# Performance work log

Measured on AMD Instinct MI355X. Metric: run time of the kernel, lower is better.

## Reference

```python
import jax, jax.numpy as jnp
import numpy as np
from jax import lax

B, N, F = 4, 8192, 64      # clouds, points per cloud, feature dim
RATIO = 0.25
M = int(N * RATIO)
K = 32                      # max_num_neighbors (torch_geometric radius default)
R = 0.1                     # ball radius (unit-cube points -> ~32 nbrs expected)
H = 64                      # MLP hidden/output width


def setup_inputs() -> dict:
    key = jax.random.key(0)
    k1, k2, k3, k4, k5, k6 = jax.random.split(key, 6)
    x = jax.random.normal(k1, (B * N, F), jnp.float32)
    pos = jax.random.uniform(k2, (B * N, 3), jnp.float32)  # unit cube
    batch = jnp.repeat(jnp.arange(B, dtype=jnp.int32), N)  # contiguous cloud ids
    s1 = 1.0 / np.sqrt(F + 3)
    W1 = jax.random.uniform(k3, (F + 3, H), jnp.float32, -s1, s1)
    b1 = jax.random.uniform(k4, (H,), jnp.float32, -s1, s1)
    s2 = 1.0 / np.sqrt(H)
    W2 = jax.random.uniform(k5, (H, H), jnp.float32, -s2, s2)
    b2 = jax.random.uniform(k6, (H,), jnp.float32, -s2, s2)
    return {"x": x, "pos": pos, "batch": batch,
            "W1": W1, "b1": b1, "W2": W2, "b2": b2}


def _fps(pc):
    """Farthest point sampling on one cloud pc [N,3] -> [M] int32 indices.
    Deterministic start at index 0 (torch_geometric uses a random start)."""
    d0 = jnp.full((N,), jnp.inf, pc.dtype)

    def step(carry, _):
        dist, last = carry
        d = jnp.sum((pc - pc[last]) ** 2, axis=-1)
        dist = jnp.minimum(dist, d)
        nxt = jnp.argmax(dist).astype(jnp.int32)
        return (dist, nxt), last

    _, idx = lax.scan(step, (d0, jnp.int32(0)), None, length=M)
    return idx


def _radius_knn(pc, centers):
    """Up-to-K neighbors of each center within radius R (nearest-first).
    Returns nbr_idx [M,K] and validity mask [M,K]."""
    d2 = jnp.sum((centers[:, None, :] - pc[None, :, :]) ** 2, axis=-1)  # [M,N]
    masked = jnp.where(d2 <= R * R, d2, jnp.inf)
    negd, idx = lax.top_k(-masked, K)
    return idx, negd > -jnp.inf


def reference(x, pos, batch, W1, b1, W2, b2):
    # batch ids are contiguous with equal-sized clouds -> reshape to [B,N,...]
    xb = x.reshape(B, N, F)
    pb = pos.reshape(B, N, 3)

    def per_cloud(xc, pc):
        samp = _fps(pc)                        # [M]   FPS indices
        centers = pc[samp]                     # [M,3]
        nbr, mask = _radius_knn(pc, centers)   # [M,K]
        # PointConv message: MLP(concat[x_j, pos_j - pos_i])
        feat = jnp.concatenate(
            [xc[nbr], pc[nbr] - centers[:, None, :]], axis=-1)  # [M,K,F+3]
        h = jax.nn.relu(feat @ W1 + b1)
        h = jax.nn.relu(h @ W2 + b2)           # [M,K,H]
        h = jnp.where(mask[..., None], h, -jnp.inf)
        out = jnp.max(h, axis=1)               # max aggregation over neighbors
        out = jnp.where(jnp.isfinite(out), out, 0.0)
        return out, centers

    out, centers = jax.vmap(per_cloud)(xb, pb)
    new_batch = jnp.repeat(jnp.arange(B, dtype=jnp.int32), M)
    return out.reshape(B * M, H), centers.reshape(B * M, 3), new_batch
```

## Files before the change

### kernel.cpp

```cpp
#include <hip/hip_runtime.h>
#include <hip/hip_bf16.h>
#include <float.h>
#include <math.h>

#define NB 4
#define NN 8192
#define FF 64
#define MM 2048
#define KK 32
#define HH 64

#define FT 512

typedef float v2f __attribute__((ext_vector_type(2)));

#define DPP_FMAX(v, ctrl, rmask)                                                \
    { int _t = __builtin_amdgcn_update_dpp((int)0xff800000, __float_as_int(v),  \
                   (ctrl), (rmask), 0xf, false);                                \
      (v) = fmaxf((v), __int_as_float(_t)); }
#define DPP_FMAX6(v)  DPP_FMAX(v,0x111,0xf) DPP_FMAX(v,0x112,0xf) \
                      DPP_FMAX(v,0x114,0xf) DPP_FMAX(v,0x118,0xf) \
                      DPP_FMAX(v,0x142,0xa) DPP_FMAX(v,0x143,0xc)

#define DPP_IMIN(v, ctrl, rmask)                                                \
    { int _t = __builtin_amdgcn_update_dpp((int)0x7fffffff, (v),                \
                   (ctrl), (rmask), 0xf, false);                                \
      (v) = min((v), _t); }
#define DPP_IMIN6(v)  DPP_IMIN(v,0x111,0xf) DPP_IMIN(v,0x112,0xf) \
                      DPP_IMIN(v,0x114,0xf) DPP_IMIN(v,0x118,0xf) \
                      DPP_IMIN(v,0x142,0xa) DPP_IMIN(v,0x143,0xc)

__global__ __launch_bounds__(FT) void fps_kernel(
    const float* __restrict__ pos,
    int* __restrict__ samp,
    float* __restrict__ centers_out,
    float* __restrict__ batch_out)
{
#pragma clang fp contract(off)
    __shared__ float4 pts4[NN];
    __shared__ float vslot[2][8];
    __shared__ int   islot[2][8];

    const int b = blockIdx.x;
    const float* pb = pos + (size_t)b * NN * 3;
    const int tid = threadIdx.x;
    const int w   = tid >> 6;
    const int lane = tid & 63;

    for (int j = tid; j < NN; j += FT)
        pts4[j] = make_float4(pb[j * 3 + 0], pb[j * 3 + 1], pb[j * 3 + 2], 0.0f);
    for (int j = tid; j < MM; j += FT) batch_out[b * MM + j] = (float)b;
    __syncthreads();

    v2f pxv[8], pyv[8], pzv[8], dv[8];
#pragma unroll
    for (int j = 0; j < 8; ++j) {
        const float4 p0 = pts4[(2 * j) * FT + tid];
        const float4 p1 = pts4[(2 * j + 1) * FT + tid];
        pxv[j] = (v2f){p0.x, p1.x};
        pyv[j] = (v2f){p0.y, p1.y};
        pzv[j] = (v2f){p0.z, p1.z};
        dv[j]  = (v2f){INFINITY, INFINITY};
    }

    int   cur = 0;
    float lx = pb[0], ly = pb[1], lz = pb[2];

    for (int s = 0; s < MM; ++s) {
#pragma clang fp contract(off)
        if (tid == 0) {
            samp[b * MM + s] = cur;
            centers_out[((size_t)b * MM + s) * 3 + 0] = lx;
            centers_out[((size_t)b * MM + s) * 3 + 1] = ly;
            centers_out[((size_t)b * MM + s) * 3 + 2] = lz;
        }
        if (s == MM - 1) break;

        const v2f l2x = (v2f){lx, lx};
        const v2f l2y = (v2f){ly, ly};
        const v2f l2z = (v2f){lz, lz};

        v2f vmax2 = (v2f){-INFINITY, -INFINITY};
#pragma unroll
        for (int j = 0; j < 8; ++j) {
            const v2f dx = pxv[j] - l2x;
            const v2f dy = pyv[j] - l2y;
            const v2f dz = pzv[j] - l2z;
            const v2f d2 = (dx * dx + dy * dy) + dz * dz;
            dv[j] = __builtin_elementwise_min(dv[j], d2);
            vmax2 = __builtin_elementwise_max(vmax2, dv[j]);
        }
        const float tv = fmaxf(vmax2.x, vmax2.y);

        float wv = tv;
        DPP_FMAX6(wv)
        const int par = s & 1;
        if (lane == 63) vslot[par][w] = wv;
        __syncthreads();

        const float4 v0 = *(const float4*)&vslot[par][0];
        const float4 v1 = *(const float4*)&vslot[par][4];
        const float V = fmaxf(fmaxf(fmaxf(v0.x, v0.y), fmaxf(v0.z, v0.w)),
                              fmaxf(fmaxf(v1.x, v1.y), fmaxf(v1.z, v1.w)));

        int cand = 0x7fffffff;
        if (tv == V) {
#pragma unroll
            for (int j = 0; j < 8; ++j) {
                if (dv[j].x == V) cand = min(cand, (2 * j) * FT + tid);
                if (dv[j].y == V) cand = min(cand, (2 * j + 1) * FT + tid);
            }
        }
        DPP_IMIN6(cand)
        if (lane == 63) islot[par][w] = cand;
        __syncthreads();

        const int4 i0 = *(const int4*)&islot[par][0];
        const int4 i1 = *(const int4*)&islot[par][4];
        cur = min(min(min(i0.x, i0.y), min(i0.z, i0.w)),
                  min(min(i1.x, i1.y), min(i1.z, i1.w)));

        const float4 wp = pts4[cur];
        lx = wp.x; ly = wp.y; lz = wp.z;
    }
}

#define CAP 256
__global__ __launch_bounds__(256) void knn_kernel(
    const float* __restrict__ pos,
    const int* __restrict__ samp,
    int* __restrict__ nbr,
    int* __restrict__ cntbuf)
{
    const int wave = threadIdx.x >> 6;
    const int lane = threadIdx.x & 63;
    const int c = blockIdx.x * 4 + wave;
    const int b = c >> 11;
    const float* pb = pos + (size_t)b * NN * 3;

    __shared__ float sd2[4][CAP];
    __shared__ int   sid[4][CAP];

    const int ctr = samp[c];
    const float cx = pb[ctr * 3 + 0];
    const float cy = pb[ctr * 3 + 1];
    const float cz = pb[ctr * 3 + 2];
    const float R2 = (float)(0.1 * 0.1);

    int cnt = 0;
    for (int r = 0; r < NN / 64; ++r) {
        const int g = r * 64 + lane;
        float dx = __fsub_rn(cx, pb[g * 3 + 0]);
        float dy = __fsub_rn(cy, pb[g * 3 + 1]);
        float dz = __fsub_rn(cz, pb[g * 3 + 2]);
        float d2 = __fadd_rn(__fadd_rn(__fmul_rn(dx, dx), __fmul_rn(dy, dy)),
                             __fmul_rn(dz, dz));
        const bool pred = (d2 <= R2);
        const unsigned long long mask = __ballot(pred);
        const int before = __popcll(mask & ((1ull << lane) - 1ull));
        if (pred) {
            const int slot = cnt + before;
            if (slot < CAP) { sd2[wave][slot] = d2; sid[wave][slot] = g; }
        }
        cnt += __popcll(mask);
    }
    if (cnt > CAP) cnt = CAP;
    __syncthreads();

    for (int ci = lane; ci < cnt; ci += 64) {
        const float dc = sd2[wave][ci];
        const int   ic = sid[wave][ci];
        int rank = 0;
        for (int j = 0; j < cnt; ++j) {
            const float dj = sd2[wave][j];
            const int   ij = sid[wave][j];
            rank += (dj < dc || (dj == dc && ij < ic)) ? 1 : 0;
        }
        if (rank < KK) nbr[c * KK + rank] = ic;
    }
    if (lane == 0) cntbuf[c] = (cnt < KK) ? cnt : KK;
}

__global__ __launch_bounds__(256) void mlp_kernel(
    const float* __restrict__ x,
    const float* __restrict__ pos,
    const float* __restrict__ W1,
    const float* __restrict__ b1,
    const float* __restrict__ W2,
    const float* __restrict__ b2,
    const int* __restrict__ nbr,
    const int* __restrict__ cntbuf,
    const float* __restrict__ centers,
    float* __restrict__ out)
{
    __shared__ float WT[64 * 68];
    __shared__ float featL[4][32 * 68];

    const int tid = threadIdx.x, wave = tid >> 6, lane = tid & 63;
    const int c = blockIdx.x * 4 + wave;
    const int b = c >> 11;
    const int cnt = cntbuf[c];

    for (int idx = tid; idx < 67 * 64; idx += 256) {
        const int i = idx >> 6, h = idx & 63;
        WT[h * 68 + i] = W1[idx];
    }
    if (tid < 64) WT[tid * 68 + 67] = 0.0f;

    const float ctr0 = centers[c * 3 + 0];
    const float ctr1 = centers[c * 3 + 1];
    const float ctr2 = centers[c * 3 + 2];
    for (int k = 0; k < cnt; ++k) {
        const int j = nbr[c * KK + k];
        featL[wave][k * 68 + lane] = x[((size_t)b * NN + j) * FF + lane];
        if (lane < 3) {
            const float pj = pos[((size_t)b * NN + j) * 3 + lane];
            const float ci = (lane == 0) ? ctr0 : ((lane == 1) ? ctr1 : ctr2);
            featL[wave][k * 68 + 64 + lane] = __fsub_rn(pj, ci);
        }
        if (lane == 3) featL[wave][k * 68 + 67] = 0.0f;
    }
    __syncthreads();

    float wreg[68];
#pragma unroll
    for (int i4 = 0; i4 < 17; ++i4) {
        const float4 v = *(const float4*)&WT[lane * 68 + i4 * 4];
        wreg[i4 * 4 + 0] = v.x; wreg[i4 * 4 + 1] = v.y;
        wreg[i4 * 4 + 2] = v.z; wreg[i4 * 4 + 3] = v.w;
    }
    const float bias1 = b1[lane];
    for (int k = 0; k < cnt; ++k) {
        float acc = bias1;
#pragma unroll
        for (int i4 = 0; i4 < 17; ++i4) {
            const float4 f = *(const float4*)&featL[wave][k * 68 + i4 * 4];
            acc = fmaf(f.x, wreg[i4 * 4 + 0], acc);
            acc = fmaf(f.y, wreg[i4 * 4 + 1], acc);
            acc = fmaf(f.z, wreg[i4 * 4 + 2], acc);
            acc = fmaf(f.w, wreg[i4 * 4 + 3], acc);
        }
        featL[wave][k * 68 + lane] = fmaxf(acc, 0.0f);
    }
    __syncthreads();

    for (int idx = tid; idx < 64 * 64; idx += 256) {
        const int i = idx >> 6, h = idx & 63;
        WT[h * 68 + i] = W2[idx];
    }
    __syncthreads();

#pragma unroll
    for (int i4 = 0; i4 < 16; ++i4) {
        const float4 v = *(const float4*)&WT[lane * 68 + i4 * 4];
        wreg[i4 * 4 + 0] = v.x; wreg[i4 * 4 + 1] = v.y;
        wreg[i4 * 4 + 2] = v.z; wreg[i4 * 4 + 3] = v.w;
    }
    const float bias2 = b2[lane];
    float m = -INFINITY;
    for (int k = 0; k < cnt; ++k) {
        float acc = bias2;
#pragma unroll
        for (int i4 = 0; i4 < 16; ++i4) {
            const float4 f = *(const float4*)&featL[wave][k * 68 + i4 * 4];
            acc = fmaf(f.x, wreg[i4 * 4 + 0], acc);
            acc = fmaf(f.y, wreg[i4 * 4 + 1], acc);
            acc = fmaf(f.z, wreg[i4 * 4 + 2], acc);
            acc = fmaf(f.w, wreg[i4 * 4 + 3], acc);
        }
        m = fmaxf(m, fmaxf(acc, 0.0f));
    }
    out[(size_t)c * HH + lane] = (cnt > 0) ? m : 0.0f;
}

extern "C" void kernel_launch(void* const* d_in, const int* in_sizes, int n_in,
                              void* d_out, int out_size, void* d_ws, size_t ws_size,
                              hipStream_t stream) {
    const float* x   = (const float*)d_in[0];
    const float* pos = (const float*)d_in[1];
    const float* W1  = (const float*)d_in[3];
    const float* b1  = (const float*)d_in[4];
    const float* W2  = (const float*)d_in[5];
    const float* b2  = (const float*)d_in[6];

    float* out         = (float*)d_out;
    float* centers_out = out + (size_t)NB * MM * HH;
    float* batch_out   = centers_out + (size_t)NB * MM * 3;

    char* ws = (char*)d_ws;
    int* samp   = (int*)ws;
    int* cntbuf = (int*)(ws + (size_t)NB * MM * 4);
    int* nbr    = (int*)(ws + (size_t)2 * NB * MM * 4);

    fps_kernel<<<NB, FT, 0, stream>>>(pos, samp, centers_out, batch_out);
    knn_kernel<<<(NB * MM) / 4, 256, 0, stream>>>(pos, samp, nbr, cntbuf);
    mlp_kernel<<<(NB * MM) / 4, 256, 0, stream>>>(x, pos, W1, b1, W2, b2,
                                                  nbr, cntbuf, centers_out, out);
}
```

Baseline: 2.123 ms.

## Fuse FPS argmax into single packed 64-bit key reduction with one barrier

Replaces the two-phase FPS argmax (max-value reduction, barrier, index-min reduction, barrier) with a single pass that packs the non-negative float distance and the inverted index into a 64-bit key. The key is reduced across the wave with DPP and across waves with an LDS atomicMax into a triple-buffered slot, leaving one __syncthreads per iteration. It also forces packed v_pk_add/v_pk_mul via inline asm for the distance update. The 64-bit DPP reduction costs twice the DPP ops per step and adds an LDS atomic, in exchange for removing a barrier from the serial 2048-step loop.

```diff
diff --git a/kernel.cpp b/kernel.cpp
--- a/kernel.cpp
+++ b/kernel.cpp
@@ -13,22 +13,33 @@
 #define FT 512
 
 typedef float v2f __attribute__((ext_vector_type(2)));
-
-#define DPP_FMAX(v, ctrl, rmask)                                                \
-    { int _t = __builtin_amdgcn_update_dpp((int)0xff800000, __float_as_int(v),  \
-                   (ctrl), (rmask), 0xf, false);                                \
-      (v) = fmaxf((v), __int_as_float(_t)); }
-#define DPP_FMAX6(v)  DPP_FMAX(v,0x111,0xf) DPP_FMAX(v,0x112,0xf) \
-                      DPP_FMAX(v,0x114,0xf) DPP_FMAX(v,0x118,0xf) \
-                      DPP_FMAX(v,0x142,0xa) DPP_FMAX(v,0x143,0xc)
-
-#define DPP_IMIN(v, ctrl, rmask)                                                \
-    { int _t = __builtin_amdgcn_update_dpp((int)0x7fffffff, (v),                \
-                   (ctrl), (rmask), 0xf, false);                                \
-      (v) = min((v), _t); }
-#define DPP_IMIN6(v)  DPP_IMIN(v,0x111,0xf) DPP_IMIN(v,0x112,0xf) \
-                      DPP_IMIN(v,0x114,0xf) DPP_IMIN(v,0x118,0xf) \
-                      DPP_IMIN(v,0x142,0xa) DPP_IMIN(v,0x143,0xc)
+typedef unsigned long long u64;
+
+__device__ __forceinline__ v2f pk_add(v2f a, v2f b) {
+    v2f r; asm("v_pk_add_f32 %0, %1, %2" : "=v"(r) : "v"(a), "v"(b)); return r;
+}
+__device__ __forceinline__ v2f pk_mul(v2f a, v2f b) {
+    v2f r; asm("v_pk_mul_f32 %0, %1, %2" : "=v"(r) : "v"(a), "v"(b)); return r;
+}
+
+#define DPP64_STEP(b, ctrl, rmask)                                              \
+    {                                                                           \
+        const unsigned int _lo = (unsigned int)(b);                             \
+        const unsigned int _hi = (unsigned int)((b) >> 32);                     \
+        const unsigned int _olo = (unsigned int)__builtin_amdgcn_update_dpp(    \
+            0, (int)_lo, (ctrl), (rmask), 0xf, false);                          \
+        const unsigned int _ohi = (unsigned int)__builtin_amdgcn_update_dpp(    \
+            0, (int)_hi, (ctrl), (rmask), 0xf, false);                          \
+        const u64 _o = (((u64)_ohi) << 32) | _olo;                              \
+        if (_o > (b)) (b) = _o;                                                 \
+    }
+#define DPP64_REDUCE(b)            \
+    DPP64_STEP(b, 0x111, 0xf)      \
+    DPP64_STEP(b, 0x112, 0xf)      \
+    DPP64_STEP(b, 0x114, 0xf)      \
+    DPP64_STEP(b, 0x118, 0xf)      \
+    DPP64_STEP(b, 0x142, 0xa)      \
+    DPP64_STEP(b, 0x143, 0xc)
 
 __global__ __launch_bounds__(FT) void fps_kernel(
     const float* __restrict__ pos,
@@ -38,18 +49,17 @@
 {
 #pragma clang fp contract(off)
     __shared__ float4 pts4[NN];
-    __shared__ float vslot[2][8];
-    __shared__ int   islot[2][8];
+    __shared__ u64 wsel[3];
 
     const int b = blockIdx.x;
     const float* pb = pos + (size_t)b * NN * 3;
     const int tid = threadIdx.x;
-    const int w   = tid >> 6;
     const int lane = tid & 63;
 
     for (int j = tid; j < NN; j += FT)
         pts4[j] = make_float4(pb[j * 3 + 0], pb[j * 3 + 1], pb[j * 3 + 2], 0.0f);
     for (int j = tid; j < MM; j += FT) batch_out[b * MM + j] = (float)b;
+    if (tid < 3) wsel[tid] = 0ull;
     __syncthreads();
 
     v2f pxv[8], pyv[8], pzv[8], dv[8];
@@ -76,50 +86,41 @@
         }
         if (s == MM - 1) break;
 
-        const v2f l2x = (v2f){lx, lx};
-        const v2f l2y = (v2f){ly, ly};
-        const v2f l2z = (v2f){lz, lz};
+        const v2f nl2x = (v2f){-lx, -lx};
+        const v2f nl2y = (v2f){-ly, -ly};
+        const v2f nl2z = (v2f){-lz, -lz};
 
         v2f vmax2 = (v2f){-INFINITY, -INFINITY};
 #pragma unroll
         for (int j = 0; j < 8; ++j) {
-            const v2f dx = pxv[j] - l2x;
-            const v2f dy = pyv[j] - l2y;
-            const v2f dz = pzv[j] - l2z;
-            const v2f d2 = (dx * dx + dy * dy) + dz * dz;
+            const v2f dx = pk_add(pxv[j], nl2x);
+            const v2f dy = pk_add(pyv[j], nl2y);
+            const v2f dz = pk_add(pzv[j], nl2z);
+            const v2f d2 = pk_add(pk_add(pk_mul(dx, dx), pk_mul(dy, dy)),
+                                  pk_mul(dz, dz));
             dv[j] = __builtin_elementwise_min(dv[j], d2);
             vmax2 = __builtin_elementwise_max(vmax2, dv[j]);
         }
         const float tv = fmaxf(vmax2.x, vmax2.y);
 
-        float wv = tv;
-        DPP_FMAX6(wv)
-        const int par = s & 1;
-        if (lane == 63) vslot[par][w] = wv;
+        int cand = 0;
+#pragma unroll
+        for (int j = 7; j >= 0; --j) {
+            cand = (dv[j].y == tv) ? (2 * j + 1) * FT + tid : cand;
+            cand = (dv[j].x == tv) ? (2 * j) * FT + tid     : cand;
+        }
+
+        u64 key = (((u64)(unsigned int)__float_as_int(tv)) << 32)
+                | (u64)(unsigned int)(8191 - cand);
+        DPP64_REDUCE(key)
+        const int sl = s % 3;
+        if (lane == 63) atomicMax(&wsel[sl], key);
         __syncthreads();
 
-        const float4 v0 = *(const float4*)&vslot[par][0];
-        const float4 v1 = *(const float4*)&vslot[par][4];
-        const float V = fmaxf(fmaxf(fmaxf(v0.x, v0.y), fmaxf(v0.z, v0.w)),
-                              fmaxf(fmaxf(v1.x, v1.y), fmaxf(v1.z, v1.w)));
-
-        int cand = 0x7fffffff;
-        if (tv == V) {
-#pragma unroll
-            for (int j = 0; j < 8; ++j) {
-                if (dv[j].x == V) cand = min(cand, (2 * j) * FT + tid);
-                if (dv[j].y == V) cand = min(cand, (2 * j + 1) * FT + tid);
-            }
-        }
-        DPP_IMIN6(cand)
-        if (lane == 63) islot[par][w] = cand;
-        __syncthreads();
-
-        const int4 i0 = *(const int4*)&islot[par][0];
-        const int4 i1 = *(const int4*)&islot[par][4];
-        cur = min(min(min(i0.x, i0.y), min(i0.z, i0.w)),
-                  min(min(i1.x, i1.y), min(i1.z, i1.w)));
-
+        const u64 win = wsel[sl];
+        if (tid == 0) wsel[(s + 2) % 3] = 0ull;
+
+        cur = 8191 - (int)(unsigned int)(win & 0xFFFFFFFFull);
         const float4 wp = pts4[cur];
         lx = wp.x; ly = wp.y; lz = wp.z;
     }
```

Result: slower. 2.241 ms (+5.6%).

## Merge FPS max and argmin reductions into a single block barrier per step

Applied to the files above, without the earlier changes.

The FPS loop now finds each wave's max distance and lowest matching index within the wave, using DPP and readlane, before any block-level step. It writes a (value, index) pair per wave and combines the pairs with a tie-aware argmax tree. This halves the number of __syncthreads per sampled point, which is the serial bottleneck of the 2048-step loop. It also switches the distance math to inline-asm packed f32 add and mul, and keeps the running min distances as scalar arrays, which risks extra register pressure or scheduling limits.

```diff
diff --git a/kernel.cpp b/kernel.cpp
--- a/kernel.cpp
+++ b/kernel.cpp
@@ -13,6 +13,13 @@
 #define FT 512
 
 typedef float v2f __attribute__((ext_vector_type(2)));
+
+__device__ __forceinline__ v2f pk_add(v2f a, v2f b) {
+    v2f r; asm("v_pk_add_f32 %0, %1, %2" : "=v"(r) : "v"(a), "v"(b)); return r;
+}
+__device__ __forceinline__ v2f pk_mul(v2f a, v2f b) {
+    v2f r; asm("v_pk_mul_f32 %0, %1, %2" : "=v"(r) : "v"(a), "v"(b)); return r;
+}
 
 #define DPP_FMAX(v, ctrl, rmask)                                                \
     { int _t = __builtin_amdgcn_update_dpp((int)0xff800000, __float_as_int(v),  \
@@ -29,6 +36,15 @@
 #define DPP_IMIN6(v)  DPP_IMIN(v,0x111,0xf) DPP_IMIN(v,0x112,0xf) \
                       DPP_IMIN(v,0x114,0xf) DPP_IMIN(v,0x118,0xf) \
                       DPP_IMIN(v,0x142,0xa) DPP_IMIN(v,0x143,0xc)
+
+__device__ __forceinline__ float readlane_f(float v, int l) {
+    return __int_as_float(__builtin_amdgcn_readlane(__float_as_int(v), l));
+}
+
+__device__ __forceinline__ float2 argmax2(float2 a, float2 b) {
+    const int ia = __float_as_int(a.y), ib = __float_as_int(b.y);
+    return (b.x > a.x || (b.x == a.x && ib < ia)) ? b : a;
+}
 
 __global__ __launch_bounds__(FT) void fps_kernel(
     const float* __restrict__ pos,
@@ -38,8 +54,7 @@
 {
 #pragma clang fp contract(off)
     __shared__ float4 pts4[NN];
-    __shared__ float vslot[2][8];
-    __shared__ int   islot[2][8];
+    __shared__ float2 slots[2][8];
 
     const int b = blockIdx.x;
     const float* pb = pos + (size_t)b * NN * 3;
@@ -52,7 +67,8 @@
     for (int j = tid; j < MM; j += FT) batch_out[b * MM + j] = (float)b;
     __syncthreads();
 
-    v2f pxv[8], pyv[8], pzv[8], dv[8];
+    v2f pxv[8], pyv[8], pzv[8];
+    float dvx[8], dvy[8];
 #pragma unroll
     for (int j = 0; j < 8; ++j) {
         const float4 p0 = pts4[(2 * j) * FT + tid];
@@ -60,7 +76,7 @@
         pxv[j] = (v2f){p0.x, p1.x};
         pyv[j] = (v2f){p0.y, p1.y};
         pzv[j] = (v2f){p0.z, p1.z};
-        dv[j]  = (v2f){INFINITY, INFINITY};
+        dvx[j] = INFINITY; dvy[j] = INFINITY;
     }
 
     int   cur = 0;
@@ -76,50 +92,54 @@
         }
         if (s == MM - 1) break;
 
-        const v2f l2x = (v2f){lx, lx};
-        const v2f l2y = (v2f){ly, ly};
-        const v2f l2z = (v2f){lz, lz};
-
-        v2f vmax2 = (v2f){-INFINITY, -INFINITY};
+        const v2f nlx = (v2f){-lx, -lx};
+        const v2f nly = (v2f){-ly, -ly};
+        const v2f nlz = (v2f){-lz, -lz};
+
 #pragma unroll
         for (int j = 0; j < 8; ++j) {
-            const v2f dx = pxv[j] - l2x;
-            const v2f dy = pyv[j] - l2y;
-            const v2f dz = pzv[j] - l2z;
-            const v2f d2 = (dx * dx + dy * dy) + dz * dz;
-            dv[j] = __builtin_elementwise_min(dv[j], d2);
-            vmax2 = __builtin_elementwise_max(vmax2, dv[j]);
-        }
-        const float tv = fmaxf(vmax2.x, vmax2.y);
+            const v2f dx = pk_add(pxv[j], nlx);
+            const v2f dy = pk_add(pyv[j], nly);
+            const v2f dz = pk_add(pzv[j], nlz);
+            const v2f d2 = pk_add(pk_add(pk_mul(dx, dx), pk_mul(dy, dy)),
+                                  pk_mul(dz, dz));
+            dvx[j] = fminf(dvx[j], d2.x);
+            dvy[j] = fminf(dvy[j], d2.y);
+        }
+        const float m0 = fmaxf(fmaxf(dvx[0], dvy[0]), fmaxf(dvx[1], dvy[1]));
+        const float m1 = fmaxf(fmaxf(dvx[2], dvy[2]), fmaxf(dvx[3], dvy[3]));
+        const float m2 = fmaxf(fmaxf(dvx[4], dvy[4]), fmaxf(dvx[5], dvy[5]));
+        const float m3 = fmaxf(fmaxf(dvx[6], dvy[6]), fmaxf(dvx[7], dvy[7]));
+        const float tv = fmaxf(fmaxf(m0, m1), fmaxf(m2, m3));
 
         float wv = tv;
         DPP_FMAX6(wv)
+        const float wmax = readlane_f(wv, 63);
+
+        int cand = 0x7fffffff;
+        if (tv == wmax) {
+#pragma unroll
+            for (int j = 7; j >= 0; --j) {
+                cand = (dvy[j] == wmax) ? (2 * j + 1) * FT + tid : cand;
+                cand = (dvx[j] == wmax) ? (2 * j) * FT + tid     : cand;
+            }
+        }
+        DPP_IMIN6(cand)
+
         const int par = s & 1;
-        if (lane == 63) vslot[par][w] = wv;
+        if (lane == 63) slots[par][w] = make_float2(wmax, __int_as_float(cand));
         __syncthreads();
 
-        const float4 v0 = *(const float4*)&vslot[par][0];
-        const float4 v1 = *(const float4*)&vslot[par][4];
-        const float V = fmaxf(fmaxf(fmaxf(v0.x, v0.y), fmaxf(v0.z, v0.w)),
-                              fmaxf(fmaxf(v1.x, v1.y), fmaxf(v1.z, v1.w)));
-
-        int cand = 0x7fffffff;
-        if (tv == V) {
-#pragma unroll
-            for (int j = 0; j < 8; ++j) {
-                if (dv[j].x == V) cand = min(cand, (2 * j) * FT + tid);
-                if (dv[j].y == V) cand = min(cand, (2 * j + 1) * FT + tid);
-            }
-        }
-        DPP_IMIN6(cand)
-        if (lane == 63) islot[par][w] = cand;
-        __syncthreads();
-
-        const int4 i0 = *(const int4*)&islot[par][0];
-        const int4 i1 = *(const int4*)&islot[par][4];
-        cur = min(min(min(i0.x, i0.y), min(i0.z, i0.w)),
-                  min(min(i1.x, i1.y), min(i1.z, i1.w)));
-
+        const float2 s0 = slots[par][0], s1 = slots[par][1];
+        const float2 s2 = slots[par][2], s3 = slots[par][3];
+        const float2 s4 = slots[par][4], s5 = slots[par][5];
+        const float2 s6 = slots[par][6], s7 = slots[par][7];
+        const float2 a0 = argmax2(s0, s1), a1 = argmax2(s2, s3);
+        const float2 a2 = argmax2(s4, s5), a3 = argmax2(s6, s7);
+        const float2 b0 = argmax2(a0, a1), b1 = argmax2(a2, a3);
+        const float2 win = argmax2(b0, b1);
+
+        cur = __float_as_int(win.y);
         const float4 wp = pts4[cur];
         lx = wp.x; ly = wp.y; lz = wp.z;
     }
```

Result: slower. 2.405 ms (+13.3%).
